# Kernel optimization log

Measured on AMD Instinct MI355X. Metric: run time of the kernel, lower is better.

The kernel has to match this reference:

```python
import jax, jax.numpy as jnp
import numpy as np
import math

DN = ('NCHW', 'OIHW', 'NCHW')

def conv3x3(x, w, b):
    # 3x3, stride 1, SAME padding conv with bias, NCHW layout
    y = jax.lax.conv_general_dilated(x, w, window_strides=(1, 1), padding='SAME', dimension_numbers=DN)
    return y + b[None, :, None, None]

def setup_inputs() -> dict:
    key = jax.random.key(0)
    ks = jax.random.split(key, 12)
    B, C, NC, S = 16, 256, 80, 4  # batch, fpn channels, num_classes, stem depth
    std = 0.01
    inp = {}
    inp['feat_p3'] = jax.random.normal(ks[0], (B, C, 64, 64), jnp.float32)
    inp['feat_p4'] = jax.random.normal(ks[1], (B, C, 32, 32), jnp.float32)
    inp['feat_p5'] = jax.random.normal(ks[2], (B, C, 16, 16), jnp.float32)
    # stem conv stacks: (S, out_c, in_c, 3, 3); all channels equal so stacking is valid
    inp['stem_cls_w'] = std * jax.random.normal(ks[3], (S, C, C, 3, 3), jnp.float32)
    inp['stem_cls_b'] = jnp.zeros((S, C), jnp.float32)
    inp['stem_box_w'] = std * jax.random.normal(ks[4], (S, C, C, 3, 3), jnp.float32)
    inp['stem_box_b'] = jnp.zeros((S, C), jnp.float32)
    inp['pred_cls_w'] = std * jax.random.normal(ks[5], (NC, C, 3, 3), jnp.float32)
    inp['pred_cls_b'] = jnp.full((NC,), -math.log(99.0), jnp.float32)  # prior-prob bias init
    inp['pred_box_w'] = std * jax.random.normal(ks[6], (4, C, 3, 3), jnp.float32)
    inp['pred_box_b'] = jnp.zeros((4,), jnp.float32)
    inp['pred_ctr_w'] = std * jax.random.normal(ks[7], (1, C, 3, 3), jnp.float32)
    inp['pred_ctr_b'] = jnp.zeros((1,), jnp.float32)
    return inp

def _flatten_hw(t):
    # (B, Ch, H, W) -> (B, H*W, Ch), channels-last as in the torch module
    B, Ch, H, W = t.shape
    return t.transpose(0, 2, 3, 1).reshape(B, H * W, Ch)

def reference(feat_p3, feat_p4, feat_p5, stem_cls_w, stem_cls_b, stem_box_w, stem_box_b,
              pred_cls_w, pred_cls_b, pred_box_w, pred_box_b, pred_ctr_w, pred_ctr_b):
    per_level = []
    for feat in (feat_p3, feat_p4, feat_p5):
        cls_feat = feat
        box_feat = feat
        for i in range(stem_cls_w.shape[0]):  # fixed small stem depth (4)
            cls_feat = jax.nn.relu(conv3x3(cls_feat, stem_cls_w[i], stem_cls_b[i]))
            box_feat = jax.nn.relu(conv3x3(box_feat, stem_box_w[i], stem_box_b[i]))
        cls_logits = conv3x3(cls_feat, pred_cls_w, pred_cls_b)   # (B, 80, H, W)
        box_deltas = conv3x3(box_feat, pred_box_w, pred_box_b)   # (B, 4, H, W)
        ctr_logits = conv3x3(box_feat, pred_ctr_w, pred_ctr_b)   # (B, 1, H, W)
        per_level.append(jnp.concatenate(
            [_flatten_hw(cls_logits), _flatten_hw(box_deltas), _flatten_hw(ctr_logits)], axis=-1))
    # concat p3/p4/p5 along location axis -> (B, 4096+1024+256, 85)
    return jnp.concatenate(per_level, axis=1)
```

## Files before the change

kernel.cpp:

```cpp
#include <hip/hip_runtime.h>


typedef __bf16 bf16;
typedef __attribute__((ext_vector_type(8))) __bf16 bf16x8;
typedef __attribute__((ext_vector_type(4))) float f32x4;

typedef unsigned int uint32_as1 __attribute__((address_space(1)));
typedef unsigned int uint32_as3 __attribute__((address_space(3)));

__device__ __forceinline__ void gl_lds16(const bf16* g, bf16* l) {
    __builtin_amdgcn_global_load_lds(
        (const uint32_as1*)(unsigned long long)g,
        (uint32_as3*)(unsigned int)(unsigned long long)l,
        16, 0, 0);
}

struct StemTab {
    const bf16* inC[3]; const bf16* inB[3];
    bf16* outC[3]; bf16* outB[3];
    int H[3]; int lw[3]; int lhw[3];
    int xend0, xend1;
};

struct PredTab {
    const bf16* inC[3]; const bf16* inB[3];
    int H[3]; int lw[3]; int lhw[3]; int offl[3];
    int xend0, xend1;
};

__global__ __launch_bounds__(256) void stem_conv_kernel(
    StemTab tab, const bf16* __restrict__ Wc, const bf16* __restrict__ Wb,
    const float* __restrict__ bc, const float* __restrict__ bb)
{
    const int bx = blockIdx.x;
    const int l  = (bx >= tab.xend0) + (bx >= tab.xend1);
    const int start = (l == 0) ? 0 : (l == 1 ? tab.xend0 : tab.xend1);
    const int local = bx - start;
    const int H = tab.H[l], lw = tab.lw[l], lhw = tab.lhw[l];

    const bf16* A; bf16* O; const bf16* BT; const float* bias;
    if (blockIdx.z == 0) { A = tab.inC[l]; O = tab.outC[l]; BT = Wc; bias = bc; }
    else                 { A = tab.inB[l]; O = tab.outB[l]; BT = Wb; bias = bb; }

    const int W   = 1 << lw;
    const int Wp  = W + 2;
    const int HW  = 1 << lhw;
    const int tid = threadIdx.x;
    const int m_base = (local >> 1) * 128;
    const int n0     = (local & 1) * 128;
    const int b   = m_base >> lhw;
    const int y0  = (m_base & (HW - 1)) >> lw;
    const int ibase = b * (H + 2) * Wp * 256;

    __shared__ __align__(16) bf16 Sh[18432];
    bf16* Als = Sh;
    bf16* Bls = Sh + 10240;

    const int ch8   = (((tid & 7) ^ ((tid >> 3) & 7)) << 3);
    const int rbase = tid >> 3;
    const int Wp256 = Wp * 256;
    const int npx   = (128 >> lw) * Wp;
    const int toff  = (128 + rbase < npx) ? 4 * 8192 : 0;
    const int ag0   = ibase + rbase * 256 + ch8;
    int bg[4];
#pragma unroll
    for (int i = 0; i < 4; ++i)
        bg[i] = (n0 + i * 32 + rbase) * 256 + ch8;

    f32x4 acc[4][4];
#pragma unroll
    for (int i = 0; i < 4; ++i)
#pragma unroll
        for (int j = 0; j < 4; ++j)
            acc[i][j] = (f32x4)(0.0f);

    const int lane = tid & 63;
    const int wv   = tid >> 6;
    const int wm   = (wv & 1) * 64;
    const int wn   = (wv >> 1) * 64;
    const int l16  = lane & 15;
    const int quad = lane >> 4;
    int pb[4];
#pragma unroll
    for (int i = 0; i < 4; ++i) {
        const int mm = wm + i * 16;
        pb[i] = mm + ((mm >> lw) << 1) + l16;
    }
    const int bRow = (wn + l16) * 64;
    const int bsw  = l16 & 7;
    bf16* lA = Als + tid * 8;
    bf16* lB = Bls + tid * 8;

    for (int dy = 0; dy < 3; ++dy) {
        const int abase = ag0 + (y0 + dy) * Wp256;
        for (int cq = 0; cq < 4; ++cq) {
            const int c0 = cq << 6;
#pragma unroll
            for (int i = 0; i < 4; ++i)
                gl_lds16(A + abase + c0 + i * 8192, lA + i * 2048);
            gl_lds16(A + abase + c0 + toff, lA + 4 * 2048);
            for (int dx = 0; dx < 3; ++dx) {
                const int boff = (dy * 3 + dx) * 65536 + c0;
#pragma unroll
                for (int i = 0; i < 4; ++i)
                    gl_lds16(BT + bg[i] + boff, lB + i * 2048);
                __syncthreads();
                int rowi[4];
#pragma unroll
                for (int i = 0; i < 4; ++i) rowi[i] = pb[i] + dx;
#pragma unroll
                for (int ks = 0; ks < 2; ++ks) {
                    const int qk = quad + ks * 4;
                    bf16x8 af[4], bfv[4];
#pragma unroll
                    for (int i = 0; i < 4; ++i)
                        af[i] = *(const bf16x8*)(Als + (rowi[i] << 6) +
                                                 ((qk ^ (rowi[i] & 7)) << 3));
#pragma unroll
                    for (int j = 0; j < 4; ++j)
                        bfv[j] = *(const bf16x8*)(Bls + bRow + j * 1024 +
                                                  ((qk ^ bsw) << 3));
#pragma unroll
                    for (int i = 0; i < 4; ++i)
#pragma unroll
                        for (int j = 0; j < 4; ++j)
                            acc[i][j] = __builtin_amdgcn_mfma_f32_16x16x32_bf16(
                                af[i], bfv[j], acc[i][j], 0, 0, 0);
                }
                __syncthreads();
            }
        }
    }

    float bv[4];
#pragma unroll
    for (int j = 0; j < 4; ++j) bv[j] = bias[n0 + wn + j * 16 + l16];
    bf16* Tw = Sh + wv * 4096;
#pragma unroll
    for (int i = 0; i < 4; ++i)
#pragma unroll
        for (int r = 0; r < 4; ++r) {
            const int row = i * 16 + quad * 4 + r;
#pragma unroll
            for (int j = 0; j < 4; ++j) {
                float v = acc[i][j][r] + bv[j];
                v = v > 0.0f ? v : 0.0f;
                const int sc = (((j * 2 + (l16 >> 3)) ^ (row & 7)) << 3) + (l16 & 7);
                Tw[row * 64 + sc] = (bf16)v;
            }
        }
    __syncthreads();
    const int rgrp = lane >> 3, cc = lane & 7;
#pragma unroll
    for (int p = 0; p < 8; ++p) {
        const int row = p * 8 + rgrp;
        bf16x8 vv = *(const bf16x8*)(Tw + row * 64 + ((cc ^ (row & 7)) << 3));
        const int ml = wm + row;
        const int y  = y0 + (ml >> lw);
        const int x  = ml & (W - 1);
        *(bf16x8*)(O + ibase + ((y + 1) * Wp + (x + 1)) * 256 + n0 + wn + cc * 8) = vv;
    }
}

__global__ __launch_bounds__(256) void pred_conv_kernel(
    PredTab tab, const bf16* __restrict__ BT, const float* __restrict__ bias,
    float* __restrict__ out)
{
    const int bx = blockIdx.x;
    const int l  = (bx >= tab.xend0) + (bx >= tab.xend1);
    const int start = (l == 0) ? 0 : (l == 1 ? tab.xend0 : tab.xend1);
    const int mt = bx - start;
    const int H = tab.H[l], lw = tab.lw[l], lhw = tab.lhw[l], off_l = tab.offl[l];
    const bf16* Ac = tab.inC[l];
    const bf16* Ab = tab.inB[l];

    const int W   = 1 << lw;
    const int Wp  = W + 2;
    const int HW  = 1 << lhw;
    const int tid = threadIdx.x;
    const int m_base = mt * 128;
    const int b   = m_base >> lhw;
    const int mi  = m_base & (HW - 1);
    const int y0  = mi >> lw;
    const int ibase = b * (H + 2) * Wp * 256;

    __shared__ __align__(16) bf16 Sh[(128 + 128 + 96) * 64];

    const int ch8   = (((tid & 7) ^ ((tid >> 3) & 7)) << 3);
    const int rbase = tid >> 3;
    int ag[4], bg[3];
#pragma unroll
    for (int i = 0; i < 4; ++i) {
        int row = i * 32 + rbase;
        int y = y0 + (row >> lw);
        int x = row & (W - 1);
        ag[i] = ibase + (y * Wp + x) * 256 + ch8;
    }
#pragma unroll
    for (int i = 0; i < 3; ++i)
        bg[i] = (i * 32 + rbase) * 256 + ch8;

    f32x4 accC[2][5], accB[2];
#pragma unroll
    for (int i = 0; i < 2; ++i) {
#pragma unroll
        for (int j = 0; j < 5; ++j) accC[i][j] = (f32x4)(0.0f);
        accB[i] = (f32x4)(0.0f);
    }

    const int lane = tid & 63;
    const int wv   = tid >> 6;
    const int l16  = lane & 15;
    const int quad = lane >> 4;
    const int xsw  = l16 & 7;
    const int aRow = (wv * 32 + l16) * 64;
    bf16* lS = Sh + tid * 8;

    for (int kc = 0; kc < 36; ++kc) {
        const int t  = kc >> 2;
        const int dy = t / 3;
        const int dx = t - dy * 3;
        const int c0 = (kc & 3) << 6;
        const int aoff = (dy * Wp + dx) * 256 + c0;
        const int boff = t * 24576 + c0;
#pragma unroll
        for (int i = 0; i < 4; ++i)
            gl_lds16(Ac + ag[i] + aoff, lS + i * 2048);
#pragma unroll
        for (int i = 0; i < 4; ++i)
            gl_lds16(Ab + ag[i] + aoff, lS + (4 + i) * 2048);
#pragma unroll
        for (int i = 0; i < 3; ++i)
            gl_lds16(BT + bg[i] + boff, lS + (8 + i) * 2048);
        __syncthreads();
#pragma unroll
        for (int ks = 0; ks < 2; ++ks) {
            const int cO = (((quad + ks * 4) ^ xsw) << 3);
            bf16x8 afc[2], afb[2], bfv[5], bfb;
#pragma unroll
            for (int i = 0; i < 2; ++i) {
                afc[i] = *(const bf16x8*)(Sh + aRow + i * 1024 + cO);
                afb[i] = *(const bf16x8*)(Sh + 8192 + aRow + i * 1024 + cO);
            }
#pragma unroll
            for (int j = 0; j < 5; ++j)
                bfv[j] = *(const bf16x8*)(Sh + 16384 + (j * 16 + l16) * 64 + cO);
            bfb = *(const bf16x8*)(Sh + 16384 + (80 + l16) * 64 + cO);
#pragma unroll
            for (int i = 0; i < 2; ++i) {
#pragma unroll
                for (int j = 0; j < 5; ++j)
                    accC[i][j] = __builtin_amdgcn_mfma_f32_16x16x32_bf16(
                        afc[i], bfv[j], accC[i][j], 0, 0, 0);
                accB[i] = __builtin_amdgcn_mfma_f32_16x16x32_bf16(
                    afb[i], bfb, accB[i], 0, 0, 0);
            }
        }
        __syncthreads();
    }

#pragma unroll
    for (int i = 0; i < 2; ++i) {
#pragma unroll
        for (int r = 0; r < 4; ++r) {
            const int ml  = wv * 32 + i * 16 + quad * 4 + r;
            const int pos = mi + ml;
            const int ob  = (b * 5376 + off_l + pos) * 85;
#pragma unroll
            for (int j = 0; j < 5; ++j)
                out[ob + j * 16 + l16] = accC[i][j][r] + bias[j * 16 + l16];
            if (l16 < 5)
                out[ob + 80 + l16] = accB[i][r] + bias[80 + l16];
        }
    }
}

__global__ void cast_pad_kernel(const float* __restrict__ in, bf16* __restrict__ out,
                                int H, int lw)
{
    const int c  = threadIdx.x;
    const int hw = blockIdx.x;
    const int b  = blockIdx.y;
    const int W  = 1 << lw;
    const int y  = hw >> lw;
    const int x  = hw & (W - 1);
    float v = in[((b * 256 + c) * H + y) * W + x];
    out[((b * (H + 2) + y + 1) * (W + 2) + (x + 1)) * 256 + c] = (bf16)v;
}

__global__ void border_zero_kernel(bf16* base, int H, size_t bufElems, int pxPerImg)
{
    const int i   = blockIdx.x;
    const int buf = blockIdx.y;
    const int c   = threadIdx.x;
    const int img = i / pxPerImg;
    const int p   = i - img * pxPerImg;
    const int Wp  = H + 2, Hp = H + 2;
    int y, xp;
    if (p < Wp)            { y = 0;      xp = p; }
    else if (p < 2 * Wp)   { y = Hp - 1; xp = p - Wp; }
    else { int q = p - 2 * Wp; y = 1 + (q >> 1); xp = (q & 1) ? (Wp - 1) : 0; }
    base[buf * bufElems + ((size_t)(img * Hp + y) * Wp + xp) * 256 + c] = (bf16)0.0f;
}

__global__ void prepack_stem_kernel(const float* __restrict__ w, bf16* __restrict__ o)
{
    const int ci = threadIdx.x;
    const int g  = blockIdx.x;
    const int co = g & 255;
    const int st = g >> 8;
    const int s  = st / 9;
    const int t  = st - s * 9;
    o[(size_t)g * 256 + ci] = (bf16)w[(((s * 256 + co) * 256 + ci) * 9) + t];
}

__global__ void prepack_pred_kernel(const float* __restrict__ wc,
                                    const float* __restrict__ wb,
                                    const float* __restrict__ wr,
                                    const float* __restrict__ cb,
                                    const float* __restrict__ bb,
                                    const float* __restrict__ br,
                                    bf16* __restrict__ oT, float* __restrict__ obias)
{
    const int ci = threadIdx.x;
    const int g  = blockIdx.x;
    const int t  = g / 96;
    const int co = g - t * 96;
    float v = 0.0f;
    if (co < 80)       v = wc[((co * 256 + ci) * 9) + t];
    else if (co < 84)  v = wb[(((co - 80) * 256 + ci) * 9) + t];
    else if (co == 84) v = wr[(ci * 9) + t];
    oT[(size_t)g * 256 + ci] = (bf16)v;
    if (g == 0 && ci < 96) {
        float bvv = 0.0f;
        if (ci < 80)       bvv = cb[ci];
        else if (ci < 84)  bvv = bb[ci - 80];
        else if (ci == 84) bvv = br[0];
        obias[ci] = bvv;
    }
}

extern "C" void kernel_launch(void* const* d_in, const int* in_sizes, int n_in,
                              void* d_out, int out_size, void* d_ws, size_t ws_size,
                              hipStream_t stream)
{
    (void)in_sizes; (void)n_in; (void)out_size;
    const float* feat[3] = {(const float*)d_in[0], (const float*)d_in[1],
                            (const float*)d_in[2]};
    const float* scw = (const float*)d_in[3];
    const float* scb = (const float*)d_in[4];
    const float* sbw = (const float*)d_in[5];
    const float* sbb = (const float*)d_in[6];
    const float* pcw = (const float*)d_in[7];
    const float* pcb = (const float*)d_in[8];
    const float* pbw = (const float*)d_in[9];
    const float* pbb = (const float*)d_in[10];
    const float* prw = (const float*)d_in[11];
    const float* prb = (const float*)d_in[12];
    float* out = (float*)d_out;

    const int Hs[3]   = {64, 32, 16};
    const int lws[3]  = {6, 5, 4};
    const int lhws[3] = {12, 10, 8};
    const int offl[3] = {0, 4096, 5120};
    const int mtiles[3] = {512, 128, 32};
    size_t bufB[3];
    for (int l = 0; l < 3; ++l)
        bufB[l] = (size_t)16 * (Hs[l] + 2) * (Hs[l] + 2) * 256 * 2;

    const size_t WSTEM = (size_t)4 * 9 * 256 * 256 * 2;
    const size_t WPRED = (size_t)9 * 96 * 256 * 2;
    const size_t FULL   = 5 * (bufB[0] + bufB[1] + bufB[2]) + 2 * WSTEM + WPRED + 384;
    const size_t SHARED = 5 * bufB[0] + 2 * WSTEM + WPRED + 384;
    if (ws_size < SHARED) return;
    const bool fused = ws_size >= FULL;

    char* ws = (char*)d_ws;
    bf16* act[3][5];
    size_t off = 0;
    if (fused) {
        for (int l = 0; l < 3; ++l)
            for (int k = 0; k < 5; ++k) { act[l][k] = (bf16*)(ws + off); off += bufB[l]; }
    } else {
        for (int k = 0; k < 5; ++k)
            for (int l = 0; l < 3; ++l) act[l][k] = (bf16*)(ws + (size_t)k * bufB[0]);
        off = 5 * bufB[0];
    }
    bf16*  wbTc = (bf16*)(ws + off); off += WSTEM;
    bf16*  wbTb = (bf16*)(ws + off); off += WSTEM;
    bf16*  pT   = (bf16*)(ws + off); off += WPRED;
    float* pB   = (float*)(ws + off);

    prepack_stem_kernel<<<dim3(9216), 256, 0, stream>>>(scw, wbTc);
    prepack_stem_kernel<<<dim3(9216), 256, 0, stream>>>(sbw, wbTb);
    prepack_pred_kernel<<<dim3(9 * 96), 256, 0, stream>>>(pcw, pbw, prw, pcb, pbb, prb,
                                                          pT, pB);

    auto launch_level_init = [&](int l) {
        const int H = Hs[l];
        const int px = 2 * (H + 2) + 2 * H;
        border_zero_kernel<<<dim3(16 * px, 5), 256, 0, stream>>>(
            act[l][0], H, bufB[l] / 2, px);
        cast_pad_kernel<<<dim3(H * H, 16), 256, 0, stream>>>(feat[l], act[l][0], H, lws[l]);
    };

    auto make_stem_tab = [&](int s, int nlev, const int* levs) {
        StemTab tb{};
        for (int i = 0; i < nlev; ++i) {
            int l = levs[i];
            tb.inC[i]  = (s == 0) ? act[l][0] : ((s & 1) ? act[l][1] : act[l][2]);
            tb.inB[i]  = (s == 0) ? act[l][0] : ((s & 1) ? act[l][3] : act[l][4]);
            tb.outC[i] = (s & 1) ? act[l][2] : act[l][1];
            tb.outB[i] = (s & 1) ? act[l][4] : act[l][3];
            tb.H[i] = Hs[l]; tb.lw[i] = lws[l]; tb.lhw[i] = lhws[l];
        }
        return tb;
    };

    if (fused) {
        for (int l = 0; l < 3; ++l) launch_level_init(l);
        const int levs[3] = {0, 1, 2};
        const int tx0 = mtiles[0] * 2, tx1 = mtiles[1] * 2, tx2 = mtiles[2] * 2;
        for (int s = 0; s < 4; ++s) {
            StemTab tb = make_stem_tab(s, 3, levs);
            tb.xend0 = tx0; tb.xend1 = tx0 + tx1;
            stem_conv_kernel<<<dim3(tx0 + tx1 + tx2, 1, 2), 256, 0, stream>>>(
                tb, wbTc + (size_t)s * 589824, wbTb + (size_t)s * 589824,
                scb + s * 256, sbb + s * 256);
        }
        PredTab pt{};
        for (int l = 0; l < 3; ++l) {
            pt.inC[l] = act[l][2]; pt.inB[l] = act[l][4];
            pt.H[l] = Hs[l]; pt.lw[l] = lws[l]; pt.lhw[l] = lhws[l]; pt.offl[l] = offl[l];
        }
        pt.xend0 = mtiles[0]; pt.xend1 = mtiles[0] + mtiles[1];
        pred_conv_kernel<<<dim3(mtiles[0] + mtiles[1] + mtiles[2]), 256, 0, stream>>>(
            pt, pT, pB, out);
    } else {
        for (int l = 0; l < 3; ++l) {
            launch_level_init(l);
            const int levs[1] = {l};
            const int tiles = mtiles[l] * 2;
            for (int s = 0; s < 4; ++s) {
                StemTab tb = make_stem_tab(s, 1, levs);
                tb.xend0 = tiles; tb.xend1 = tiles;
                stem_conv_kernel<<<dim3(tiles, 1, 2), 256, 0, stream>>>(
                    tb, wbTc + (size_t)s * 589824, wbTb + (size_t)s * 589824,
                    scb + s * 256, sbb + s * 256);
            }
            PredTab pt{};
            pt.inC[0] = act[l][2]; pt.inB[0] = act[l][4];
            pt.H[0] = Hs[l]; pt.lw[0] = lws[l]; pt.lhw[0] = lhws[l]; pt.offl[0] = offl[l];
            pt.xend0 = mtiles[l]; pt.xend1 = mtiles[l];
            pred_conv_kernel<<<dim3(mtiles[l]), 256, 0, stream>>>(pt, pT, pB, out);
        }
    }
}
```

Measured before the change: 1.114 ms.

## Widen stem conv tiles to full channel width, reuse halo across taps, batch aux kernels

The stem conv block now runs 512 threads and covers all 256 output channels per 128-pixel tile. The input halo for all three dy rows is loaded once per channel chunk and reused across all nine taps, instead of being reloaded for each dy. This is meant to cut redundant activation loads and halve the number of A-tile fetches per output channel. Separately, cast_pad is rewritten to use coalesced, LDS-transposed row writes; border zeroing and cast run as single multi-level launches; and the three prepack kernels are merged into one. In exchange, LDS use doubles, which may lower occupancy, and register pressure rises under the 512-thread launch bound.

```diff
diff --git a/kernel.cpp b/kernel.cpp
--- a/kernel.cpp
+++ b/kernel.cpp
@@ -21,14 +21,22 @@
     int H[3]; int lw[3]; int lhw[3];
     int xend0, xend1;
 };
-
 struct PredTab {
     const bf16* inC[3]; const bf16* inB[3];
     int H[3]; int lw[3]; int lhw[3]; int offl[3];
     int xend0, xend1;
 };
-
-__global__ __launch_bounds__(256) void stem_conv_kernel(
+struct CastTab {
+    const float* in[3]; bf16* out[3];
+    int H[3]; int lw[3];
+    int xend0, xend1;
+};
+struct BZTab {
+    bf16* base[3]; int H[3]; size_t bufE[3]; int ppi[3];
+    int xend0, xend1;
+};
+
+__global__ __launch_bounds__(512, 4) void stem_conv_kernel(
     StemTab tab, const bf16* __restrict__ Wc, const bf16* __restrict__ Wb,
     const float* __restrict__ bc, const float* __restrict__ bb)
 {
@@ -46,26 +54,28 @@
     const int Wp  = W + 2;
     const int HW  = 1 << lhw;
     const int tid = threadIdx.x;
-    const int m_base = (local >> 1) * 128;
-    const int n0     = (local & 1) * 128;
+    const int m_base = local * 128;
     const int b   = m_base >> lhw;
     const int y0  = (m_base & (HW - 1)) >> lw;
     const int ibase = b * (H + 2) * Wp * 256;
 
-    __shared__ __align__(16) bf16 Sh[18432];
+    __shared__ __align__(16) bf16 Sh[36864];
     bf16* Als = Sh;
-    bf16* Bls = Sh + 10240;
-
-    const int ch8   = (((tid & 7) ^ ((tid >> 3) & 7)) << 3);
+    bf16* Bls = Sh + 20480;
+
     const int rbase = tid >> 3;
+    const int ch8   = (((tid & 7) ^ (rbase & 7)) << 3);
+    const int npx   = ((128 >> lw) + 2) * Wp;
     const int Wp256 = Wp * 256;
-    const int npx   = (128 >> lw) * Wp;
-    const int toff  = (128 + rbase < npx) ? 4 * 8192 : 0;
-    const int ag0   = ibase + rbase * 256 + ch8;
+    const int ag0   = ibase + y0 * Wp256 + rbase * 256 + ch8;
+    int aoffs[5];
+#pragma unroll
+    for (int i = 0; i < 5; ++i)
+        aoffs[i] = (i * 64 + rbase < npx) ? i * 16384 : 0;
     int bg[4];
 #pragma unroll
     for (int i = 0; i < 4; ++i)
-        bg[i] = (n0 + i * 32 + rbase) * 256 + ch8;
+        bg[i] = (i * 64 + rbase) * 256 + ch8;
 
     f32x4 acc[4][4];
 #pragma unroll
@@ -84,38 +94,36 @@
 #pragma unroll
     for (int i = 0; i < 4; ++i) {
         const int mm = wm + i * 16;
-        pb[i] = mm + ((mm >> lw) << 1) + l16;
+        pb[i] = mm + l16 + ((mm >> lw) << 1);
     }
     const int bRow = (wn + l16) * 64;
     const int bsw  = l16 & 7;
     bf16* lA = Als + tid * 8;
     bf16* lB = Bls + tid * 8;
 
-    for (int dy = 0; dy < 3; ++dy) {
-        const int abase = ag0 + (y0 + dy) * Wp256;
-        for (int cq = 0; cq < 4; ++cq) {
-            const int c0 = cq << 6;
-#pragma unroll
-            for (int i = 0; i < 4; ++i)
-                gl_lds16(A + abase + c0 + i * 8192, lA + i * 2048);
-            gl_lds16(A + abase + c0 + toff, lA + 4 * 2048);
+    for (int cq = 0; cq < 4; ++cq) {
+        const int c0 = cq << 6;
+#pragma unroll
+        for (int i = 0; i < 5; ++i)
+            gl_lds16(A + ag0 + c0 + aoffs[i], lA + i * 4096);
+        for (int dy = 0; dy < 3; ++dy) {
             for (int dx = 0; dx < 3; ++dx) {
-                const int boff = (dy * 3 + dx) * 65536 + c0;
+                const int boff = ((dy * 3 + dx) << 16) + c0;
 #pragma unroll
                 for (int i = 0; i < 4; ++i)
-                    gl_lds16(BT + bg[i] + boff, lB + i * 2048);
+                    gl_lds16(BT + bg[i] + boff, lB + i * 4096);
                 __syncthreads();
-                int rowi[4];
-#pragma unroll
-                for (int i = 0; i < 4; ++i) rowi[i] = pb[i] + dx;
+                const int rb0 = dy * Wp + dx;
 #pragma unroll
                 for (int ks = 0; ks < 2; ++ks) {
                     const int qk = quad + ks * 4;
                     bf16x8 af[4], bfv[4];
 #pragma unroll
-                    for (int i = 0; i < 4; ++i)
-                        af[i] = *(const bf16x8*)(Als + (rowi[i] << 6) +
-                                                 ((qk ^ (rowi[i] & 7)) << 3));
+                    for (int i = 0; i < 4; ++i) {
+                        const int rr = pb[i] + rb0;
+                        af[i] = *(const bf16x8*)(Als + (rr << 6) +
+                                                 ((qk ^ (rr & 7)) << 3));
+                    }
 #pragma unroll
                     for (int j = 0; j < 4; ++j)
                         bfv[j] = *(const bf16x8*)(Bls + bRow + j * 1024 +
@@ -134,7 +142,7 @@
 
     float bv[4];
 #pragma unroll
-    for (int j = 0; j < 4; ++j) bv[j] = bias[n0 + wn + j * 16 + l16];
+    for (int j = 0; j < 4; ++j) bv[j] = bias[wn + j * 16 + l16];
     bf16* Tw = Sh + wv * 4096;
 #pragma unroll
     for (int i = 0; i < 4; ++i)
@@ -158,7 +166,7 @@
         const int ml = wm + row;
         const int y  = y0 + (ml >> lw);
         const int x  = ml & (W - 1);
-        *(bf16x8*)(O + ibase + ((y + 1) * Wp + (x + 1)) * 256 + n0 + wn + cc * 8) = vv;
+        *(bf16x8*)(O + ibase + ((y + 1) * Wp + (x + 1)) * 256 + wn + cc * 8) = vv;
     }
 }
 
@@ -275,68 +283,98 @@
     }
 }
 
-__global__ void cast_pad_kernel(const float* __restrict__ in, bf16* __restrict__ out,
-                                int H, int lw)
+__global__ __launch_bounds__(256) void cast_pad_kernel(CastTab tb)
 {
-    const int c  = threadIdx.x;
-    const int hw = blockIdx.x;
-    const int b  = blockIdx.y;
-    const int W  = 1 << lw;
-    const int y  = hw >> lw;
-    const int x  = hw & (W - 1);
-    float v = in[((b * 256 + c) * H + y) * W + x];
-    out[((b * (H + 2) + y + 1) * (W + 2) + (x + 1)) * 256 + c] = (bf16)v;
-}
-
-__global__ void border_zero_kernel(bf16* base, int H, size_t bufElems, int pxPerImg)
+    const int bx = blockIdx.x;
+    const int l  = (bx >= tb.xend0) + (bx >= tb.xend1);
+    const int start = (l == 0) ? 0 : (l == 1 ? tb.xend0 : tb.xend1);
+    const int job = bx - start;
+    const int H = tb.H[l], lw = tb.lw[l];
+    const int W = 1 << lw, Wp = W + 2;
+    const int b = job >> lw;
+    const int y = job & (W - 1);
+    const float* in = tb.in[l] + ((size_t)(b * 256) * H + y) * W;
+    bf16* out = tb.out[l] + ((size_t)(b * (H + 2) + y + 1) * Wp + 1) * 256;
+    const int tid = threadIdx.x;
+    __shared__ bf16 L[16384];
+    const int cpp = 256 >> lw;
+    const int x = tid & (W - 1);
+    const int cb0 = tid >> lw;
+    for (int p = 0; p < W; ++p) {
+        const int c = p * cpp + cb0;
+        float v = in[(size_t)c * H * W + x];
+        L[x * 256 + ((((c >> 3) ^ (x & 31))) << 3) + (c & 7)] = (bf16)v;
+    }
+    __syncthreads();
+    const int wpass = W >> 3;
+    for (int q = 0; q < wpass; ++q) {
+        const int id = q * 256 + tid;
+        const int xo = id >> 5;
+        const int k  = id & 31;
+        bf16x8 vv = *(const bf16x8*)(L + xo * 256 + ((k ^ (xo & 31)) << 3));
+        *(bf16x8*)(out + xo * 256 + k * 8) = vv;
+    }
+}
+
+__global__ void border_zero_kernel(BZTab tb)
 {
-    const int i   = blockIdx.x;
+    const int bx = blockIdx.x;
+    const int l  = (bx >= tb.xend0) + (bx >= tb.xend1);
+    const int start = (l == 0) ? 0 : (l == 1 ? tb.xend0 : tb.xend1);
+    const int i   = bx - start;
     const int buf = blockIdx.y;
     const int c   = threadIdx.x;
-    const int img = i / pxPerImg;
-    const int p   = i - img * pxPerImg;
+    const int H = tb.H[l];
+    const int ppi = tb.ppi[l];
+    const int img = i / ppi;
+    const int p   = i - img * ppi;
     const int Wp  = H + 2, Hp = H + 2;
     int y, xp;
     if (p < Wp)            { y = 0;      xp = p; }
     else if (p < 2 * Wp)   { y = Hp - 1; xp = p - Wp; }
     else { int q = p - 2 * Wp; y = 1 + (q >> 1); xp = (q & 1) ? (Wp - 1) : 0; }
-    base[buf * bufElems + ((size_t)(img * Hp + y) * Wp + xp) * 256 + c] = (bf16)0.0f;
-}
-
-__global__ void prepack_stem_kernel(const float* __restrict__ w, bf16* __restrict__ o)
+    tb.base[l][buf * tb.bufE[l] + ((size_t)(img * Hp + y) * Wp + xp) * 256 + c]
+        = (bf16)0.0f;
+}
+
+__global__ void prepack_kernel(const float* __restrict__ scw,
+                               const float* __restrict__ sbw,
+                               const float* __restrict__ pcw,
+                               const float* __restrict__ pbw,
+                               const float* __restrict__ prw,
+                               const float* __restrict__ pcb,
+                               const float* __restrict__ pbb,
+                               const float* __restrict__ prb,
+                               bf16* __restrict__ wc, bf16* __restrict__ wb,
+                               bf16* __restrict__ pT, float* __restrict__ pB)
 {
     const int ci = threadIdx.x;
-    const int g  = blockIdx.x;
-    const int co = g & 255;
-    const int st = g >> 8;
-    const int s  = st / 9;
-    const int t  = st - s * 9;
-    o[(size_t)g * 256 + ci] = (bf16)w[(((s * 256 + co) * 256 + ci) * 9) + t];
-}
-
-__global__ void prepack_pred_kernel(const float* __restrict__ wc,
-                                    const float* __restrict__ wb,
-                                    const float* __restrict__ wr,
-                                    const float* __restrict__ cb,
-                                    const float* __restrict__ bb,
-                                    const float* __restrict__ br,
-                                    bf16* __restrict__ oT, float* __restrict__ obias)
-{
-    const int ci = threadIdx.x;
-    const int g  = blockIdx.x;
-    const int t  = g / 96;
-    const int co = g - t * 96;
-    float v = 0.0f;
-    if (co < 80)       v = wc[((co * 256 + ci) * 9) + t];
-    else if (co < 84)  v = wb[(((co - 80) * 256 + ci) * 9) + t];
-    else if (co == 84) v = wr[(ci * 9) + t];
-    oT[(size_t)g * 256 + ci] = (bf16)v;
-    if (g == 0 && ci < 96) {
-        float bvv = 0.0f;
-        if (ci < 80)       bvv = cb[ci];
-        else if (ci < 84)  bvv = bb[ci - 80];
-        else if (ci == 84) bvv = br[0];
-        obias[ci] = bvv;
+    int g = blockIdx.x;
+    if (g < 18432) {
+        const float* w = (g < 9216) ? scw : sbw;
+        bf16* o        = (g < 9216) ? wc  : wb;
+        if (g >= 9216) g -= 9216;
+        const int co = g & 255;
+        const int st = g >> 8;
+        const int s  = st / 9;
+        const int t  = st - s * 9;
+        o[(size_t)g * 256 + ci] = (bf16)w[(((s * 256 + co) * 256 + ci) * 9) + t];
+    } else {
+        g -= 18432;
+        const int t  = g / 96;
+        const int co = g - t * 96;
+        float v = 0.0f;
+        if (co < 80)       v = pcw[((co * 256 + ci) * 9) + t];
+        else if (co < 84)  v = pbw[(((co - 80) * 256 + ci) * 9) + t];
+        else if (co == 84) v = prw[(ci * 9) + t];
+        pT[(size_t)g * 256 + ci] = (bf16)v;
+        if (g == 0 && ci < 96) {
+            float bvv = 0.0f;
+            if (ci < 80)       bvv = pcb[ci];
+            else if (ci < 84)  bvv = pbb[ci - 80];
+            else if (ci == 84) bvv = prb[0];
+            pB[ci] = bvv;
+        }
     }
 }
 
@@ -391,18 +429,9 @@
     bf16*  pT   = (bf16*)(ws + off); off += WPRED;
     float* pB   = (float*)(ws + off);
 
-    prepack_stem_kernel<<<dim3(9216), 256, 0, stream>>>(scw, wbTc);
-    prepack_stem_kernel<<<dim3(9216), 256, 0, stream>>>(sbw, wbTb);
-    prepack_pred_kernel<<<dim3(9 * 96), 256, 0, stream>>>(pcw, pbw, prw, pcb, pbb, prb,
-                                                          pT, pB);
-
-    auto launch_level_init = [&](int l) {
-        const int H = Hs[l];
-        const int px = 2 * (H + 2) + 2 * H;
-        border_zero_kernel<<<dim3(16 * px, 5), 256, 0, stream>>>(
-            act[l][0], H, bufB[l] / 2, px);
-        cast_pad_kernel<<<dim3(H * H, 16), 256, 0, stream>>>(feat[l], act[l][0], H, lws[l]);
-    };
+    prepack_kernel<<<dim3(19296), 256, 0, stream>>>(scw, sbw, pcw, pbw, prw,
+                                                    pcb, pbb, prb,
+                                                    wbTc, wbTb, pT, pB);
 
     auto make_stem_tab = [&](int s, int nlev, const int* levs) {
         StemTab tb{};
@@ -418,13 +447,31 @@
     };
 
     if (fused) {
-        for (int l = 0; l < 3; ++l) launch_level_init(l);
+        BZTab bz{};
+        int bpx[3];
+        for (int l = 0; l < 3; ++l) {
+            bz.base[l] = act[l][0]; bz.H[l] = Hs[l]; bz.bufE[l] = bufB[l] / 2;
+            bpx[l] = 2 * (Hs[l] + 2) + 2 * Hs[l];
+            bz.ppi[l] = bpx[l];
+        }
+        bz.xend0 = 16 * bpx[0]; bz.xend1 = bz.xend0 + 16 * bpx[1];
+        const int bztot = bz.xend1 + 16 * bpx[2];
+        border_zero_kernel<<<dim3(bztot, 5), 256, 0, stream>>>(bz);
+
+        CastTab ct{};
+        for (int l = 0; l < 3; ++l) {
+            ct.in[l] = feat[l]; ct.out[l] = act[l][0];
+            ct.H[l] = Hs[l]; ct.lw[l] = lws[l];
+        }
+        ct.xend0 = 16 * Hs[0]; ct.xend1 = ct.xend0 + 16 * Hs[1];
+        cast_pad_kernel<<<dim3(ct.xend1 + 16 * Hs[2]), 256, 0, stream>>>(ct);
+
         const int levs[3] = {0, 1, 2};
-        const int tx0 = mtiles[0] * 2, tx1 = mtiles[1] * 2, tx2 = mtiles[2] * 2;
+        const int tx0 = mtiles[0], tx1 = mtiles[1], tx2 = mtiles[2];
         for (int s = 0; s < 4; ++s) {
             StemTab tb = make_stem_tab(s, 3, levs);
             tb.xend0 = tx0; tb.xend1 = tx0 + tx1;
-            stem_conv_kernel<<<dim3(tx0 + tx1 + tx2, 1, 2), 256, 0, stream>>>(
+            stem_conv_kernel<<<dim3(tx0 + tx1 + tx2, 1, 2), 512, 0, stream>>>(
                 tb, wbTc + (size_t)s * 589824, wbTb + (size_t)s * 589824,
                 scb + s * 256, sbb + s * 256);
         }
@@ -438,13 +485,22 @@
             pt, pT, pB, out);
     } else {
         for (int l = 0; l < 3; ++l) {
-            launch_level_init(l);
+            const int bpx = 2 * (Hs[l] + 2) + 2 * Hs[l];
+            BZTab bz{};
+            bz.base[0] = act[l][0]; bz.H[0] = Hs[l]; bz.bufE[0] = bufB[0] / 2;
+            bz.ppi[0] = bpx; bz.xend0 = 16 * bpx; bz.xend1 = 16 * bpx;
+            border_zero_kernel<<<dim3(16 * bpx, 5), 256, 0, stream>>>(bz);
+            CastTab ct{};
+            ct.in[0] = feat[l]; ct.out[0] = act[l][0];
+            ct.H[0] = Hs[l]; ct.lw[0] = lws[l];
+            ct.xend0 = 16 * Hs[l]; ct.xend1 = 16 * Hs[l];
+            cast_pad_kernel<<<dim3(16 * Hs[l]), 256, 0, stream>>>(ct);
+
             const int levs[1] = {l};
-            const int tiles = mtiles[l] * 2;
             for (int s = 0; s < 4; ++s) {
                 StemTab tb = make_stem_tab(s, 1, levs);
-                tb.xend0 = tiles; tb.xend1 = tiles;
-                stem_conv_kernel<<<dim3(tiles, 1, 2), 256, 0, stream>>>(
+                tb.xend0 = mtiles[l]; tb.xend1 = mtiles[l];
+                stem_conv_kernel<<<dim3(mtiles[l], 1, 2), 512, 0, stream>>>(
                     tb, wbTc + (size_t)s * 589824, wbTb + (size_t)s * 589824,
                     scb + s * 256, sbb + s * 256);
             }
```

Result: slower. 1.690 ms (+51.7%).
